# Kernel tuning notes

Measured on AMD Instinct MI355X. Metric: run time of the kernel, lower is better.

## Reference

```python
import jax, jax.numpy as jnp
import numpy as np


def setup_inputs() -> dict:
    key = jax.random.key(0)
    k1, k2 = jax.random.split(key)
    B, L, D = 16, 512, 256
    text_features = jax.random.normal(k1, (B, L, D), dtype=jnp.float32)
    durations = jax.random.randint(k2, (B, L), 0, 32, dtype=jnp.int64)
    return {"text_features": text_features, "durations": durations, "target_length": 8192}


def reference(text_features, durations, target_length):
    """Length-regulator: expand [B,L,d] phoneme features to [B,T,d] frames.

    Frame t of batch b copies phoneme p where cumsum(dur)[b,p-1] <= t < cumsum(dur)[b,p];
    frames past the total duration are zero (matches torch zeros-init + trim/pad to
    target_length, since padding with the last frame only occurs when the buffer was
    already target_length long in the original code path with target_length set).
    """
    B, L, D = text_features.shape
    T = target_length  # static python int -> jit-friendly fixed output length
    cum = jnp.cumsum(durations, axis=1)                      # [B, L]
    t = jnp.arange(T, dtype=cum.dtype)                       # [T]
    # first phoneme index p with cum[b,p] > t  (side='right')
    idx = jax.vmap(lambda c: jnp.searchsorted(c, t, side='right'))(cum)  # [B, T]
    idx = jnp.minimum(idx, L - 1)
    valid = t[None, :] < cum[:, -1:]                         # [B, T] frames within total dur
    gathered = jnp.take_along_axis(text_features, idx[:, :, None], axis=1)  # [B, T, D]
    return jnp.where(valid[:, :, None], gathered, jnp.zeros((), dtype=text_features.dtype))
```

## Files before the change

### kernel.cpp

```cpp
#include <hip/hip_runtime.h>

#define MAX_L 2048
#define MAX_EPC 8
#define FPB 128

__global__ __launch_bounds__(256) void lr_index_kernel(
        const int* __restrict__ dur,
        const int* __restrict__ tlen,
        int* __restrict__ gmap,
        int BL, int BT) {
    const int T = *tlen;
    const int B = BT / T;
    const int L = BL / B;

    __shared__ int sc[MAX_L];
    __shared__ int swsum[4];

    const int tid  = threadIdx.x;
    const int lane = tid & 63;
    const int wv   = tid >> 6;

    for (int b = blockIdx.x; b < B; b += gridDim.x) {
        __syncthreads();

        const int epc  = (L + blockDim.x - 1) / blockDim.x;
        const int base = tid * epc;
        const int* __restrict__ drow = dur + (size_t)b * L;
        int local[MAX_EPC];
        int run = 0;
#pragma unroll
        for (int e = 0; e < MAX_EPC; ++e) {
            int v = 0;
            if (e < epc && base + e < L) v = drow[base + e];
            run += v;
            local[e] = run;
        }
        int wsum = run;
#pragma unroll
        for (int off = 1; off < 64; off <<= 1) {
            int up = __shfl_up(wsum, off, 64);
            if (lane >= off) wsum += up;
        }
        if (lane == 63) swsum[wv] = wsum;
        __syncthreads();
        int wprefix = 0;
        for (int w = 0; w < wv; ++w) wprefix += swsum[w];
        const int chunk_prefix = wprefix + wsum - run;
#pragma unroll
        for (int e = 0; e < MAX_EPC; ++e)
            if (e < epc && base + e < L) sc[base + e] = chunk_prefix + local[e];
        __syncthreads();

        const int total_raw = sc[L - 1];
        const int total = total_raw < T ? total_raw : T;
        int* __restrict__ gm = gmap + (size_t)b * T;

        for (int p = tid; p < L; p += blockDim.x) {
            int s = p ? sc[p - 1] : 0;
            int e = sc[p];
            if (s > T) s = T;
            if (e > T) e = T;
            const int g = b * L + p;
            for (int t = s; t < e; ++t) gm[t] = g;
        }
        for (int t = total + tid; t < T; t += blockDim.x) gm[t] = -1;
    }
}

__global__ __launch_bounds__(256) void lr_copy_kernel(
        const float* __restrict__ feat,
        const int* __restrict__ gmap,
        float* __restrict__ out,
        int BT, int vecs) {
    const long fb = (long)blockIdx.x * FPB;
    if (fb >= BT) return;

    const int tid  = threadIdx.x;
    const int lane = tid & 63;
    const int wv   = tid >> 6;
    const int nf   = (int)(((long)BT - fb) < FPB ? ((long)BT - fb) : (long)FPB);

    if (nf == FPB && vecs == 64) {
        const long f0 = fb + (long)wv * 32;
        const int si = gmap[f0 + (lane & 31)];
        const float4* __restrict__ fv = (const float4*)feat;
        float4* __restrict__ op = (float4*)out + (size_t)f0 * 64 + lane;
        int prev = -2;
        float4 v = make_float4(0.f, 0.f, 0.f, 0.f);
#pragma unroll
        for (int j = 0; j < 32; ++j) {
            const int g = __builtin_amdgcn_readlane(si, j);
            if (g != prev) {
                v = (g >= 0) ? fv[(size_t)g * 64 + lane]
                             : make_float4(0.f, 0.f, 0.f, 0.f);
                prev = g;
            }
            op[(size_t)j * 64] = v;
        }
    } else {
        const float4 z = make_float4(0.f, 0.f, 0.f, 0.f);
        for (int f = wv; f < nf; f += 4) {
            const int g = gmap[fb + f];
            float4* __restrict__ orow = (float4*)out + (size_t)(fb + f) * vecs;
            if (g >= 0) {
                const float4* __restrict__ irow =
                    (const float4*)feat + (size_t)g * vecs;
                for (int i = lane; i < vecs; i += 64) orow[i] = irow[i];
            } else {
                for (int i = lane; i < vecs; i += 64) orow[i] = z;
            }
        }
    }
}

__global__ __launch_bounds__(256) void lr_fused_kernel(
        const float* __restrict__ feat,
        const int* __restrict__ dur,
        const int* __restrict__ tlen,
        float* __restrict__ out,
        int BL, int BT, int D) {
    const int T = *tlen;
    const int B = BT / T;
    const int L = BL / B;
    const int vecs = D >> 2;

    __shared__ int sc[MAX_L];
    __shared__ int swsum[4];
    __shared__ int sidx[FPB];

    const long frame_base0 = (long)blockIdx.x * FPB;
    if (frame_base0 >= BT) return;

    const int tid  = threadIdx.x;
    const int lane = tid & 63;
    const int wv   = tid >> 6;

    long fb_ = frame_base0;
    int remaining = (int)((long)BT - frame_base0 < FPB ? (long)BT - frame_base0
                                                       : (long)FPB);

    while (remaining > 0) {
        const int b   = (int)(fb_ / T);
        const int tt0 = (int)(fb_ - (long)b * T);
        const int seg = remaining < (T - tt0) ? remaining : (T - tt0);

        __syncthreads();
        const int epc  = (L + blockDim.x - 1) / blockDim.x;
        const int base = tid * epc;
        const int* __restrict__ drow = dur + (size_t)b * L;
        int local[MAX_EPC];
        int run = 0;
#pragma unroll
        for (int e = 0; e < MAX_EPC; ++e) {
            int v = 0;
            if (e < epc && base + e < L) v = drow[base + e];
            run += v;
            local[e] = run;
        }
        int wsum = run;
#pragma unroll
        for (int off = 1; off < 64; off <<= 1) {
            int up = __shfl_up(wsum, off, 64);
            if (lane >= off) wsum += up;
        }
        if (lane == 63) swsum[wv] = wsum;
        __syncthreads();
        int wprefix = 0;
        for (int w = 0; w < wv; ++w) wprefix += swsum[w];
        const int chunk_prefix = wprefix + wsum - run;
#pragma unroll
        for (int e = 0; e < MAX_EPC; ++e)
            if (e < epc && base + e < L) sc[base + e] = chunk_prefix + local[e];
        __syncthreads();

        const int total = sc[L - 1];

        if (tid < seg) {
            const int t = tt0 + tid;
            int p = -1;
            if (t < total) {
                int lo = 0, hi = L - 1;
                while (lo < hi) {
                    const int mid = (lo + hi) >> 1;
                    if (sc[mid] > t) hi = mid;
                    else             lo = mid + 1;
                }
                p = lo;
            }
            sidx[tid] = p;
        }
        __syncthreads();

        if (seg == FPB && vecs == 64) {
            const float4* __restrict__ fbp =
                (const float4*)feat + (size_t)b * L * 64;
            float4* __restrict__ op =
                (float4*)out + ((size_t)fb_ + (size_t)wv * 32) * 64 + lane;
            const int si = sidx[wv * 32 + (lane & 31)];
            int prev = -2;
            float4 v = make_float4(0.f, 0.f, 0.f, 0.f);
#pragma unroll
            for (int j = 0; j < 32; ++j) {
                const int p = __builtin_amdgcn_readlane(si, j);
                if (p != prev) {
                    v = (p >= 0) ? fbp[(size_t)p * 64 + lane]
                                 : make_float4(0.f, 0.f, 0.f, 0.f);
                    prev = p;
                }
                op[(size_t)j * 64] = v;
            }
        } else {
            const float4* __restrict__ fbp =
                (const float4*)feat + (size_t)b * L * vecs;
            const float4 z = make_float4(0.f, 0.f, 0.f, 0.f);
            for (int f = wv; f < seg; f += 4) {
                const int p = sidx[f];
                float4* __restrict__ orow = (float4*)out + ((size_t)fb_ + f) * vecs;
                if (p >= 0) {
                    const float4* __restrict__ irow = fbp + (size_t)p * vecs;
                    for (int i = lane; i < vecs; i += 64) orow[i] = irow[i];
                } else {
                    for (int i = lane; i < vecs; i += 64) orow[i] = z;
                }
            }
        }

        fb_ += seg;
        remaining -= seg;
    }
}

extern "C" void kernel_launch(void* const* d_in, const int* in_sizes, int n_in,
                              void* d_out, int out_size, void* d_ws, size_t ws_size,
                              hipStream_t stream) {
    const float* feat = (const float*)d_in[0];
    const int*   dur  = (const int*)d_in[1];
    const int*   tlen = (const int*)d_in[2];

    const int BL = in_sizes[1];
    const int D  = in_sizes[0] / in_sizes[1];
    const int BT = out_size / D;

    const int grid = (BT + FPB - 1) / FPB;

    if (ws_size >= (size_t)BT * sizeof(int)) {
        lr_index_kernel<<<64, 256, 0, stream>>>(dur, tlen, (int*)d_ws, BL, BT);
        lr_copy_kernel<<<grid, 256, 0, stream>>>(feat, (int*)d_ws,
                                                 (float*)d_out, BT, D >> 2);
    } else {
        lr_fused_kernel<<<grid, 256, 0, stream>>>(feat, dur, tlen, (float*)d_out,
                                                  BL, BT, D);
    }
}
```

Measured before the change: 149.1 us.

## Split index map build across time slices with binary search; branchless gather loads

The index kernel now divides each batch row into 16 time slices, one per work item, and launches 256 blocks instead of 64. Each frame finds its phoneme by binary search over the shared cumsum, replacing the per-phoneme serial write loop, which suffered load imbalance with up to 32 frames per thread. Each block still recomputes the full prefix sum for its row. The copy loops also drop the cached-value branch and issue an unconditional clamped load for every frame, masking invalid frames to zero. This adds redundant reads of feature rows, which should mostly hit in cache, in exchange for independent loads that can overlap.

```diff
diff --git a/kernel.cpp b/kernel.cpp
--- a/kernel.cpp
+++ b/kernel.cpp
@@ -3,6 +3,7 @@
 #define MAX_L 2048
 #define MAX_EPC 8
 #define FPB 128
+#define SB  16
 
 __global__ __launch_bounds__(256) void lr_index_kernel(
         const int* __restrict__ dur,
@@ -20,7 +21,13 @@
     const int lane = tid & 63;
     const int wv   = tid >> 6;
 
-    for (int b = blockIdx.x; b < B; b += gridDim.x) {
+    const int nwork = B * SB;
+    const int slen  = (T + SB - 1) / SB;
+
+    for (int w = blockIdx.x; w < nwork; w += gridDim.x) {
+        const int b  = w / SB;
+        const int sl = w - b * SB;
+
         __syncthreads();
 
         const int epc  = (L + blockDim.x - 1) / blockDim.x;
@@ -44,26 +51,31 @@
         if (lane == 63) swsum[wv] = wsum;
         __syncthreads();
         int wprefix = 0;
-        for (int w = 0; w < wv; ++w) wprefix += swsum[w];
+        for (int ww = 0; ww < wv; ++ww) wprefix += swsum[ww];
         const int chunk_prefix = wprefix + wsum - run;
 #pragma unroll
         for (int e = 0; e < MAX_EPC; ++e)
             if (e < epc && base + e < L) sc[base + e] = chunk_prefix + local[e];
         __syncthreads();
 
-        const int total_raw = sc[L - 1];
-        const int total = total_raw < T ? total_raw : T;
+        const int total = sc[L - 1];
         int* __restrict__ gm = gmap + (size_t)b * T;
 
-        for (int p = tid; p < L; p += blockDim.x) {
-            int s = p ? sc[p - 1] : 0;
-            int e = sc[p];
-            if (s > T) s = T;
-            if (e > T) e = T;
-            const int g = b * L + p;
-            for (int t = s; t < e; ++t) gm[t] = g;
-        }
-        for (int t = total + tid; t < T; t += blockDim.x) gm[t] = -1;
+        const int t0 = sl * slen;
+        const int t1 = (t0 + slen) < T ? (t0 + slen) : T;
+        for (int t = t0 + tid; t < t1; t += blockDim.x) {
+            int g = -1;
+            if (t < total) {
+                int lo = 0, hi = L - 1;
+                while (lo < hi) {
+                    const int mid = (lo + hi) >> 1;
+                    if (sc[mid] > t) hi = mid;
+                    else             lo = mid + 1;
+                }
+                g = b * L + lo;
+            }
+            gm[t] = g;
+        }
     }
 }
 
@@ -85,16 +97,12 @@
         const int si = gmap[f0 + (lane & 31)];
         const float4* __restrict__ fv = (const float4*)feat;
         float4* __restrict__ op = (float4*)out + (size_t)f0 * 64 + lane;
-        int prev = -2;
-        float4 v = make_float4(0.f, 0.f, 0.f, 0.f);
 #pragma unroll
         for (int j = 0; j < 32; ++j) {
-            const int g = __builtin_amdgcn_readlane(si, j);
-            if (g != prev) {
-                v = (g >= 0) ? fv[(size_t)g * 64 + lane]
-                             : make_float4(0.f, 0.f, 0.f, 0.f);
-                prev = g;
-            }
+            const int g  = __builtin_amdgcn_readlane(si, j);
+            const int gc = g < 0 ? 0 : g;
+            float4 v = fv[(size_t)gc * 64 + lane];
+            if (g < 0) v = make_float4(0.f, 0.f, 0.f, 0.f);
             op[(size_t)j * 64] = v;
         }
     } else {
@@ -197,16 +205,12 @@
             float4* __restrict__ op =
                 (float4*)out + ((size_t)fb_ + (size_t)wv * 32) * 64 + lane;
             const int si = sidx[wv * 32 + (lane & 31)];
-            int prev = -2;
-            float4 v = make_float4(0.f, 0.f, 0.f, 0.f);
 #pragma unroll
             for (int j = 0; j < 32; ++j) {
-                const int p = __builtin_amdgcn_readlane(si, j);
-                if (p != prev) {
-                    v = (p >= 0) ? fbp[(size_t)p * 64 + lane]
-                                 : make_float4(0.f, 0.f, 0.f, 0.f);
-                    prev = p;
-                }
+                const int p  = __builtin_amdgcn_readlane(si, j);
+                const int pc = p < 0 ? 0 : p;
+                float4 v = fbp[(size_t)pc * 64 + lane];
+                if (p < 0) v = make_float4(0.f, 0.f, 0.f, 0.f);
                 op[(size_t)j * 64] = v;
             }
         } else {
@@ -244,7 +248,7 @@
     const int grid = (BT + FPB - 1) / FPB;
 
     if (ws_size >= (size_t)BT * sizeof(int)) {
-        lr_index_kernel<<<64, 256, 0, stream>>>(dur, tlen, (int*)d_ws, BL, BT);
+        lr_index_kernel<<<256, 256, 0, stream>>>(dur, tlen, (int*)d_ws, BL, BT);
         lr_copy_kernel<<<grid, 256, 0, stream>>>(feat, (int*)d_ws,
                                                  (float*)d_out, BT, D >> 2);
     } else {
```

Result: no change. 147.4 us (-1.1%).
